# Kernel tuning notes

Hardware: AMD Instinct MI355X
Metric: run time of the kernel (lower is better)

Reference implementation:

```python
import jax, jax.numpy as jnp
import numpy as np

N_SEGMENTS = 50000  # number of destination nodes (index values in [0, N_SEGMENTS))


def setup_inputs() -> dict:
    key = jax.random.key(0)
    k1, k2 = jax.random.split(key)
    input = jax.random.normal(k1, (1600000, 64), dtype=jnp.float32)
    index = jax.random.randint(k2, (1600000,), 0, N_SEGMENTS, dtype=jnp.int64)
    return {"input": input, "index": index}


def reference(input, index):
    # Sum-aggregate rows of `input` grouped by `index`: out[n] = sum_{e: index[e]==n} input[e]
    # Equivalent to the custom loma_sum_aggr forward (scatter-add segmented reduction).
    return jax.ops.segment_sum(input, index, num_segments=N_SEGMENTS)
```

## Files before the change

kernel.cpp:

```cpp
#include <hip/hip_runtime.h>

#define N_SEGMENTS 50000
#define N_ROWS     1600000
#define N_FEAT     64
#define SCHUNK     1000
#define N_CHUNKS   50

typedef float f32x4 __attribute__((ext_vector_type(4)));

__global__ void seg_sum_atomic(const float* __restrict__ in,
                               const int*   __restrict__ idx,
                               float*       __restrict__ out) {
    long long t   = (long long)blockIdx.x * blockDim.x + threadIdx.x;
    long long row = t >> 6;
    int       c   = (int)(t & 63);
    if (row < (long long)N_ROWS) {
        int s = idx[row];
        float v = in[row * N_FEAT + c];
        atomicAdd(out + (long long)s * N_FEAT + c, v);
    }
}

__global__ void hist_kernel(const int* __restrict__ idx, int* __restrict__ cnt) {
    int t = blockIdx.x * blockDim.x + threadIdx.x;
    int r = t << 2;
    if (r < N_ROWS) {
        int4 v = *reinterpret_cast<const int4*>(idx + r);
        atomicAdd(&cnt[v.x], 1);
        atomicAdd(&cnt[v.y], 1);
        atomicAdd(&cnt[v.z], 1);
        atomicAdd(&cnt[v.w], 1);
    }
}

__global__ void __launch_bounds__(1024) scan_part(const int* __restrict__ cnt,
                                                  int* __restrict__ base,
                                                  int* __restrict__ cursor,
                                                  int* __restrict__ csum) {
    __shared__ int part[1024];
    int b = blockIdx.x;
    int t = threadIdx.x;
    int g = b * SCHUNK + t;
    part[t] = (t < SCHUNK) ? cnt[g] : 0;
    __syncthreads();
    for (int ofs = 1; ofs < 1024; ofs <<= 1) {
        int u = (t >= ofs) ? part[t - ofs] : 0;
        __syncthreads();
        part[t] += u;
        __syncthreads();
    }
    int excl = (t == 0) ? 0 : part[t - 1];
    if (t < SCHUNK) { base[g] = excl; cursor[g] = excl; }
    if (t == 1023) csum[b] = part[1023];
}

__global__ void scan_fix(const int* __restrict__ csum,
                         int* __restrict__ off,
                         int* __restrict__ base) {
    int t = threadIdx.x;
    int orig = (t < N_CHUNKS) ? csum[t] : 0;
    int v = orig;
    for (int ofs = 1; ofs < 64; ofs <<= 1) {
        int u = __shfl_up(v, ofs);
        if (t >= ofs) v += u;
    }
    if (t < N_CHUNKS) off[t] = v - orig;
    if (t == N_CHUNKS - 1) { off[N_CHUNKS] = v; base[N_SEGMENTS] = 0; }
}

__global__ void scatter_kernel(const int* __restrict__ idx,
                               int* __restrict__ cursor,
                               const int* __restrict__ off,
                               int* __restrict__ rowids) {
    int t = blockIdx.x * blockDim.x + threadIdx.x;
    int r = t << 2;
    if (r < N_ROWS) {
        int4 v = *reinterpret_cast<const int4*>(idx + r);
        rowids[atomicAdd(&cursor[v.x], 1) + off[v.x / SCHUNK]] = r;
        rowids[atomicAdd(&cursor[v.y], 1) + off[v.y / SCHUNK]] = r + 1;
        rowids[atomicAdd(&cursor[v.z], 1) + off[v.z / SCHUNK]] = r + 2;
        rowids[atomicAdd(&cursor[v.w], 1) + off[v.w / SCHUNK]] = r + 3;
    }
}

__device__ __forceinline__ f32x4 fadd4(f32x4 a, f32x4 b) { return a + b; }

__global__ void gather_kernel(const float* __restrict__ in,
                              const int*   __restrict__ rowids,
                              const int*   __restrict__ base,
                              const int*   __restrict__ off,
                              float*       __restrict__ out) {
    int wave = (blockIdx.x * blockDim.x + threadIdx.x) >> 6;
    int lane = threadIdx.x & 63;
    if (wave >= N_SEGMENTS) return;
    int q = lane >> 4;
    int f = lane & 15;
    int beg = base[wave]     + off[wave / SCHUNK];
    int end = base[wave + 1] + off[(wave + 1) / SCHUNK];
    f32x4 z = {0.f, 0.f, 0.f, 0.f};
    f32x4 a0 = z, a1 = z, a2 = z, a3 = z;

    for (int j0 = beg; j0 < end; j0 += 64) {
        int n = end - j0; if (n > 64) n = 64;
        int myid = (lane < n) ? rowids[j0 + lane] : 0;
#pragma unroll
        for (int k = 0; k < 64; k += 16) {
            int i0 = k + q, i1 = k + 4 + q, i2 = k + 8 + q, i3 = k + 12 + q;
            int r0 = __shfl(myid, i0 < n ? i0 : 0);
            int r1 = __shfl(myid, i1 < n ? i1 : 0);
            int r2 = __shfl(myid, i2 < n ? i2 : 0);
            int r3 = __shfl(myid, i3 < n ? i3 : 0);
            f32x4 v0 = __builtin_nontemporal_load(
                reinterpret_cast<const f32x4*>(in + (long long)r0 * N_FEAT + f * 4));
            f32x4 v1 = __builtin_nontemporal_load(
                reinterpret_cast<const f32x4*>(in + (long long)r1 * N_FEAT + f * 4));
            f32x4 v2 = __builtin_nontemporal_load(
                reinterpret_cast<const f32x4*>(in + (long long)r2 * N_FEAT + f * 4));
            f32x4 v3 = __builtin_nontemporal_load(
                reinterpret_cast<const f32x4*>(in + (long long)r3 * N_FEAT + f * 4));
            if (i0 < n) a0 = fadd4(a0, v0);
            if (i1 < n) a1 = fadd4(a1, v1);
            if (i2 < n) a2 = fadd4(a2, v2);
            if (i3 < n) a3 = fadd4(a3, v3);
        }
    }

    f32x4 a = fadd4(fadd4(a0, a1), fadd4(a2, a3));
    a.x += __shfl_xor(a.x, 16); a.y += __shfl_xor(a.y, 16);
    a.z += __shfl_xor(a.z, 16); a.w += __shfl_xor(a.w, 16);
    a.x += __shfl_xor(a.x, 32); a.y += __shfl_xor(a.y, 32);
    a.z += __shfl_xor(a.z, 32); a.w += __shfl_xor(a.w, 32);

    if (q == 0) {
        __builtin_nontemporal_store(a,
            reinterpret_cast<f32x4*>(out + (size_t)wave * N_FEAT + f * 4));
    }
}

extern "C" void kernel_launch(void* const* d_in, const int* in_sizes, int n_in,
                              void* d_out, int out_size, void* d_ws, size_t ws_size,
                              hipStream_t stream) {
    const float* in  = (const float*)d_in[0];
    const int*   idx = (const int*)d_in[1];
    float*       out = (float*)d_out;

    const size_t need = ((size_t)N_SEGMENTS * 3 + 1 + 128 + N_ROWS) * sizeof(int);
    if (ws_size < need) {
        (void)hipMemsetAsync(d_out, 0, (size_t)out_size * sizeof(float), stream);
        const long long total = (long long)N_ROWS * N_FEAT;
        const int block = 256;
        const long long grid = (total + block - 1) / block;
        seg_sum_atomic<<<(unsigned)grid, block, 0, stream>>>(in, idx, out);
        return;
    }

    int* cnt    = (int*)d_ws;
    int* base   = cnt + N_SEGMENTS;
    int* cursor = base + N_SEGMENTS + 1;
    int* csum   = cursor + N_SEGMENTS;
    int* off    = csum + 64;
    int* rowids = off + 64;

    (void)hipMemsetAsync(cnt, 0, (size_t)N_SEGMENTS * sizeof(int), stream);

    const int block = 256;
    const int gridRows = (N_ROWS / 4 + block - 1) / block;
    hist_kernel   <<<gridRows, block, 0, stream>>>(idx, cnt);
    scan_part     <<<N_CHUNKS, 1024, 0, stream>>>(cnt, base, cursor, csum);
    scan_fix      <<<1, 64, 0, stream>>>(csum, off, base);
    scatter_kernel<<<gridRows, block, 0, stream>>>(idx, cursor, off, rowids);

    const int gridGather = (N_SEGMENTS * 64) / 256;
    gather_kernel <<<gridGather, block, 0, stream>>>(in, rowids, base, off, out);
}
```

Measured before the change: 705.5 us.

## Fuse counting-sort pipeline into one cooperative kernel with grid syncs

Replaces the memset plus five separate launches (histogram, two-level scan, scatter, gather) with a single cooperative kernel. Stages are separated by grid.sync and work is spread over a persistent grid sized from occupancy. The per-chunk scan now uses 256 threads with four elements each, rowid stores are non-temporal, and the gather skips empty 16-row sub-batches. This removes launch gaps and per-kernel ramp up and tail, at the cost of grid-wide barriers and fewer resident waves for the memory-bound gather phase.

```diff
diff --git a/kernel.cpp b/kernel.cpp
--- a/kernel.cpp
+++ b/kernel.cpp
@@ -1,10 +1,14 @@
 #include <hip/hip_runtime.h>
+#include <hip/hip_cooperative_groups.h>
+
+namespace cg = cooperative_groups;
 
 #define N_SEGMENTS 50000
 #define N_ROWS     1600000
 #define N_FEAT     64
 #define SCHUNK     1000
 #define N_CHUNKS   50
+#define COOP_TPB   256
 
 typedef float f32x4 __attribute__((ext_vector_type(4)));
 
@@ -82,8 +86,6 @@
         rowids[atomicAdd(&cursor[v.w], 1) + off[v.w / SCHUNK]] = r + 3;
     }
 }
-
-__device__ __forceinline__ f32x4 fadd4(f32x4 a, f32x4 b) { return a + b; }
 
 __global__ void gather_kernel(const float* __restrict__ in,
                               const int*   __restrict__ rowids,
@@ -118,14 +120,14 @@
                 reinterpret_cast<const f32x4*>(in + (long long)r2 * N_FEAT + f * 4));
             f32x4 v3 = __builtin_nontemporal_load(
                 reinterpret_cast<const f32x4*>(in + (long long)r3 * N_FEAT + f * 4));
-            if (i0 < n) a0 = fadd4(a0, v0);
-            if (i1 < n) a1 = fadd4(a1, v1);
-            if (i2 < n) a2 = fadd4(a2, v2);
-            if (i3 < n) a3 = fadd4(a3, v3);
-        }
-    }
-
-    f32x4 a = fadd4(fadd4(a0, a1), fadd4(a2, a3));
+            if (i0 < n) a0 += v0;
+            if (i1 < n) a1 += v1;
+            if (i2 < n) a2 += v2;
+            if (i3 < n) a3 += v3;
+        }
+    }
+
+    f32x4 a = (a0 + a1) + (a2 + a3);
     a.x += __shfl_xor(a.x, 16); a.y += __shfl_xor(a.y, 16);
     a.z += __shfl_xor(a.z, 16); a.w += __shfl_xor(a.w, 16);
     a.x += __shfl_xor(a.x, 32); a.y += __shfl_xor(a.y, 32);
@@ -134,6 +136,140 @@
     if (q == 0) {
         __builtin_nontemporal_store(a,
             reinterpret_cast<f32x4*>(out + (size_t)wave * N_FEAT + f * 4));
+    }
+}
+
+__global__ void __launch_bounds__(COOP_TPB) fused_pipeline(
+        const float* __restrict__ in,
+        const int*   __restrict__ idx,
+        int* __restrict__ cnt,
+        int* __restrict__ base,
+        int* __restrict__ cursor,
+        int* __restrict__ csum,
+        int* __restrict__ off,
+        int* __restrict__ rowids,
+        float* __restrict__ out)
+{
+    cg::grid_group grid = cg::this_grid();
+    __shared__ int part[COOP_TPB];
+
+    const int tid      = threadIdx.x;
+    const int gtid     = blockIdx.x * COOP_TPB + tid;
+    const int nthreads = gridDim.x * COOP_TPB;
+
+    for (int i = gtid; i < N_SEGMENTS; i += nthreads) cnt[i] = 0;
+    grid.sync();
+
+    for (int u = gtid; u < N_ROWS / 4; u += nthreads) {
+        int4 v = *reinterpret_cast<const int4*>(idx + (u << 2));
+        atomicAdd(&cnt[v.x], 1);
+        atomicAdd(&cnt[v.y], 1);
+        atomicAdd(&cnt[v.z], 1);
+        atomicAdd(&cnt[v.w], 1);
+    }
+    grid.sync();
+
+    if (blockIdx.x < N_CHUNKS) {
+        const int b = blockIdx.x;
+        int e0 = 0, e1 = 0, e2 = 0, e3 = 0, s = 0;
+        if (tid < 250) {
+            const int g = b * SCHUNK + (tid << 2);
+            e0 = cnt[g]; e1 = cnt[g + 1]; e2 = cnt[g + 2]; e3 = cnt[g + 3];
+            s = e0 + e1 + e2 + e3;
+        }
+        part[tid] = s;
+        __syncthreads();
+        for (int ofs = 1; ofs < COOP_TPB; ofs <<= 1) {
+            int u = (tid >= ofs) ? part[tid - ofs] : 0;
+            __syncthreads();
+            part[tid] += u;
+            __syncthreads();
+        }
+        if (tid < 250) {
+            int run = (tid == 0) ? 0 : part[tid - 1];
+            const int g = b * SCHUNK + (tid << 2);
+            base[g]     = run; cursor[g]     = run; run += e0;
+            base[g + 1] = run; cursor[g + 1] = run; run += e1;
+            base[g + 2] = run; cursor[g + 2] = run; run += e2;
+            base[g + 3] = run; cursor[g + 3] = run;
+        }
+        if (tid == COOP_TPB - 1) csum[b] = part[COOP_TPB - 1];
+    }
+    grid.sync();
+
+    if (blockIdx.x == 0 && tid < 64) {
+        int orig = (tid < N_CHUNKS) ? csum[tid] : 0;
+        int v = orig;
+        for (int ofs = 1; ofs < 64; ofs <<= 1) {
+            int u = __shfl_up(v, ofs);
+            if (tid >= ofs) v += u;
+        }
+        if (tid < N_CHUNKS) off[tid] = v - orig;
+        if (tid == N_CHUNKS - 1) { off[N_CHUNKS] = v; base[N_SEGMENTS] = 0; }
+    }
+    grid.sync();
+
+    for (int u = gtid; u < N_ROWS / 4; u += nthreads) {
+        const int r = u << 2;
+        int4 v = *reinterpret_cast<const int4*>(idx + r);
+        int p0 = atomicAdd(&cursor[v.x], 1) + off[v.x / SCHUNK];
+        int p1 = atomicAdd(&cursor[v.y], 1) + off[v.y / SCHUNK];
+        int p2 = atomicAdd(&cursor[v.z], 1) + off[v.z / SCHUNK];
+        int p3 = atomicAdd(&cursor[v.w], 1) + off[v.w / SCHUNK];
+        __builtin_nontemporal_store(r,     rowids + p0);
+        __builtin_nontemporal_store(r + 1, rowids + p1);
+        __builtin_nontemporal_store(r + 2, rowids + p2);
+        __builtin_nontemporal_store(r + 3, rowids + p3);
+    }
+    grid.sync();
+
+    const int lane = tid & 63;
+    const int q = lane >> 4;
+    const int f = lane & 15;
+    const int wstride = nthreads >> 6;
+    for (int w = (gtid >> 6); w < N_SEGMENTS; w += wstride) {
+        int beg = base[w]     + off[w / SCHUNK];
+        int end = base[w + 1] + off[(w + 1) / SCHUNK];
+        f32x4 z = {0.f, 0.f, 0.f, 0.f};
+        f32x4 a0 = z, a1 = z, a2 = z, a3 = z;
+
+        for (int j0 = beg; j0 < end; j0 += 64) {
+            int n = end - j0; if (n > 64) n = 64;
+            int myid = rowids[j0 + lane];
+#pragma unroll
+            for (int k = 0; k < 64; k += 16) {
+                if (k < n) {
+                    int i0 = k + q, i1 = k + 4 + q, i2 = k + 8 + q, i3 = k + 12 + q;
+                    int r0 = __shfl(myid, i0 < n ? i0 : 0);
+                    int r1 = __shfl(myid, i1 < n ? i1 : 0);
+                    int r2 = __shfl(myid, i2 < n ? i2 : 0);
+                    int r3 = __shfl(myid, i3 < n ? i3 : 0);
+                    f32x4 v0 = __builtin_nontemporal_load(
+                        reinterpret_cast<const f32x4*>(in + (long long)r0 * N_FEAT + f * 4));
+                    f32x4 v1 = __builtin_nontemporal_load(
+                        reinterpret_cast<const f32x4*>(in + (long long)r1 * N_FEAT + f * 4));
+                    f32x4 v2 = __builtin_nontemporal_load(
+                        reinterpret_cast<const f32x4*>(in + (long long)r2 * N_FEAT + f * 4));
+                    f32x4 v3 = __builtin_nontemporal_load(
+                        reinterpret_cast<const f32x4*>(in + (long long)r3 * N_FEAT + f * 4));
+                    if (i0 < n) a0 += v0;
+                    if (i1 < n) a1 += v1;
+                    if (i2 < n) a2 += v2;
+                    if (i3 < n) a3 += v3;
+                }
+            }
+        }
+
+        f32x4 a = (a0 + a1) + (a2 + a3);
+        a.x += __shfl_xor(a.x, 16); a.y += __shfl_xor(a.y, 16);
+        a.z += __shfl_xor(a.z, 16); a.w += __shfl_xor(a.w, 16);
+        a.x += __shfl_xor(a.x, 32); a.y += __shfl_xor(a.y, 32);
+        a.z += __shfl_xor(a.z, 32); a.w += __shfl_xor(a.w, 32);
+
+        if (q == 0) {
+            __builtin_nontemporal_store(a,
+                reinterpret_cast<f32x4*>(out + (size_t)w * N_FEAT + f * 4));
+        }
     }
 }
 
@@ -144,7 +280,7 @@
     const int*   idx = (const int*)d_in[1];
     float*       out = (float*)d_out;
 
-    const size_t need = ((size_t)N_SEGMENTS * 3 + 1 + 128 + N_ROWS) * sizeof(int);
+    const size_t need = ((size_t)N_SEGMENTS * 3 + 1 + 128 + N_ROWS + 64) * sizeof(int);
     if (ws_size < need) {
         (void)hipMemsetAsync(d_out, 0, (size_t)out_size * sizeof(float), stream);
         const long long total = (long long)N_ROWS * N_FEAT;
@@ -161,15 +297,31 @@
     int* off    = csum + 64;
     int* rowids = off + 64;
 
+    static int coop_blocks = 0;
+    if (coop_blocks == 0) {
+        int maxb = 0;
+        if (hipOccupancyMaxActiveBlocksPerMultiprocessor(
+                &maxb, fused_pipeline, COOP_TPB, 0) != hipSuccess || maxb <= 0)
+            maxb = 4;
+        coop_blocks = maxb * 256;
+        if (coop_blocks > 2048) coop_blocks = 2048;
+    }
+
+    void* args[] = { (void*)&in, (void*)&idx, (void*)&cnt, (void*)&base,
+                     (void*)&cursor, (void*)&csum, (void*)&off,
+                     (void*)&rowids, (void*)&out };
+    hipError_t err = hipLaunchCooperativeKernel((const void*)fused_pipeline,
+                                                dim3(coop_blocks), dim3(COOP_TPB),
+                                                args, 0, stream);
+    if (err == hipSuccess) return;
+
     (void)hipMemsetAsync(cnt, 0, (size_t)N_SEGMENTS * sizeof(int), stream);
-
     const int block = 256;
     const int gridRows = (N_ROWS / 4 + block - 1) / block;
     hist_kernel   <<<gridRows, block, 0, stream>>>(idx, cnt);
     scan_part     <<<N_CHUNKS, 1024, 0, stream>>>(cnt, base, cursor, csum);
     scan_fix      <<<1, 64, 0, stream>>>(csum, off, base);
     scatter_kernel<<<gridRows, block, 0, stream>>>(idx, cursor, off, rowids);
-
     const int gridGather = (N_SEGMENTS * 64) / 256;
     gather_kernel <<<gridGather, block, 0, stream>>>(in, rowids, base, off, out);
 }
```

Result: slower. 1.068 ms (+51.4%).
